# Kernel optimization log

Measured on AMD Instinct MI355X. Metric: run time of the kernel, lower is better.

## Reference

```python
import jax, jax.numpy as jnp
import numpy as np

B, S, D = 4, 2048, 1024
H, DK, DV = 16, 64, 64
EPS = 1e-6


def setup_inputs() -> dict:
    key = jax.random.key(0)
    ks = jax.random.split(key, 7)
    sc = 0.02
    return {
        "q": jax.random.normal(ks[0], (B, S, D), jnp.float32),
        "k": jax.random.normal(ks[1], (B, S, D), jnp.float32),
        "v": jax.random.normal(ks[2], (B, S, D), jnp.float32),
        "Wq": jax.random.normal(ks[3], (D, H * DK), jnp.float32) * sc,
        "Wk": jax.random.normal(ks[4], (D, H * DK), jnp.float32) * sc,
        "Wv": jax.random.normal(ks[5], (D, H * DV), jnp.float32) * sc,
        "Wo": jax.random.normal(ks[6], (H * DV, D), jnp.float32) * sc,
        "ln_gamma": jnp.ones((D,), jnp.float32),
        "ln_beta": jnp.zeros((D,), jnp.float32),
    }


def reference(q, k, v, Wq, Wk, Wv, Wo, ln_gamma, ln_beta):
    residual = q
    # QKV projections -> [b, h, s, d]
    qh = (q @ Wq).reshape(B, S, H, DK).transpose(0, 2, 1, 3)
    kh = (k @ Wk).reshape(B, S, H, DK).transpose(0, 2, 1, 3)
    vh = (v @ Wv).reshape(B, S, H, DV).transpose(0, 2, 1, 3)
    temperature = jnp.sqrt(jnp.float32(DK))
    # scaled dot-product attention (reverse=False, dropout = eval identity)
    scores = jnp.einsum('bhqd,bhkd->bhqk', qh / temperature, kh)
    attn = jax.nn.softmax(scores, axis=-1)
    ctx = jnp.einsum('bhqk,bhkd->bhqd', attn, vh)
    # merge heads and output projection
    ctx = ctx.transpose(0, 2, 1, 3).reshape(B, S, H * DV)
    out = ctx @ Wo + residual
    # LayerNorm eps=1e-6
    mu = out.mean(-1, keepdims=True)
    var = out.var(-1, keepdims=True)
    out = (out - mu) / jnp.sqrt(var + EPS) * ln_gamma + ln_beta
    return out
```

## Files before the change

kernel.cpp:

```cpp
#include <hip/hip_runtime.h>

typedef __bf16 bf16x8 __attribute__((ext_vector_type(8)));
typedef __bf16 bf16x4 __attribute__((ext_vector_type(4)));
typedef float  f32x4  __attribute__((ext_vector_type(4)));

#define MFMA16(a, b, c) __builtin_amdgcn_mfma_f32_16x16x32_bf16(a, b, c, 0, 0, 0)
#define AS1(p) ((__attribute__((address_space(1))) void*)(p))
#define AS3(p) ((__attribute__((address_space(3))) void*)(p))

union U8 { uint u[4]; bf16x8 v; };
union U4 { bf16x4 h[2]; bf16x8 v; };

__device__ inline uint packbf(float a, float b) {
  union { __bf16 h[2]; uint u; } x;
  x.h[0] = (__bf16)a; x.h[1] = (__bf16)b; return x.u;
}

__device__ inline float fast_exp2(float x) {
  float r;
  asm("v_exp_f32 %0, %1" : "=v"(r) : "v"(x));
  return r;
}

__global__ __launch_bounds__(256) void cvt3_kernel(const float* __restrict__ q,
                                                   const float* __restrict__ k,
                                                   const float* __restrict__ v,
                                                   __bf16* __restrict__ out, int n4) {
  const int z = blockIdx.y;
  const float* in = z == 0 ? q : (z == 1 ? k : v);
  int i = blockIdx.x * blockDim.x + threadIdx.x;
  if (i < n4) {
    float4 vv = ((const float4*)in)[i];
    bf16x4 o = {(__bf16)vv.x, (__bf16)vv.y, (__bf16)vv.z, (__bf16)vv.w};
    *(bf16x4*)(out + (size_t)z * n4 * 4 + (size_t)i * 4) = o;
  }
}

__global__ void wtrans_kernel(const float* __restrict__ in, __bf16* __restrict__ out) {
  __shared__ __bf16 t[64][65];
  int bx = blockIdx.x * 64, by = blockIdx.y * 64;
  int tx = threadIdx.x;
  for (int ty = threadIdx.y; ty < 64; ty += 4)
    t[ty][tx] = (__bf16)in[(size_t)(by + ty) * 1024 + bx + tx];
  __syncthreads();
  for (int ty = threadIdx.y; ty < 64; ty += 4)
    out[(size_t)(bx + ty) * 1024 + by + tx] = t[tx][ty];
}

__global__ __launch_bounds__(256) void gemm_qkv_kernel(
    const __bf16* __restrict__ A0, const __bf16* __restrict__ B0, __bf16* __restrict__ C0,
    const __bf16* __restrict__ A1, const __bf16* __restrict__ B1, __bf16* __restrict__ C1,
    const __bf16* __restrict__ A2, const __bf16* __restrict__ B2, __bf16* __restrict__ C2) {
  __shared__ __bf16 As[128 * 32];
  __shared__ __bf16 Bs[128 * 32];
  const int z = blockIdx.z;
  const __bf16* A = z == 0 ? A0 : (z == 1 ? A1 : A2);
  const __bf16* BT = z == 0 ? B0 : (z == 1 ? B1 : B2);
  __bf16* Cb = z == 0 ? C0 : (z == 1 ? C1 : C2);
  const int K = 1024, N = 1024;
  const int t = threadIdx.x, l = t & 63, w = t >> 6;
  const int lr = l & 15, lg = l >> 4;
  const int brow = blockIdx.y * 128, bcol = blockIdx.x * 128;
  const int wr = w >> 1, wc = w & 1;
  f32x4 acc[4][4] = {};

  const int srow = w * 16 + (l >> 2);
  const int scol = (l & 3) * 8;
  const __bf16* Ag = A + (size_t)(brow + srow) * K + scol;
  const __bf16* Bg = BT + (size_t)(bcol + srow) * K + scol;
  __bf16* Asw = As + w * 512;
  __bf16* Bsw = Bs + w * 512;

  for (int k0 = 0; k0 < K; k0 += 32) {
    __builtin_amdgcn_global_load_lds(AS1(Ag + k0), AS3(Asw), 16, 0, 0);
    __builtin_amdgcn_global_load_lds(AS1(Ag + k0 + (size_t)64 * K), AS3(Asw + 2048), 16, 0, 0);
    __builtin_amdgcn_global_load_lds(AS1(Bg + k0), AS3(Bsw), 16, 0, 0);
    __builtin_amdgcn_global_load_lds(AS1(Bg + k0 + (size_t)64 * K), AS3(Bsw + 2048), 16, 0, 0);
    __syncthreads();
    bf16x8 a[4], b[4];
#pragma unroll
    for (int m = 0; m < 4; ++m)
      a[m] = *(const bf16x8*)(As + (wr * 64 + m * 16 + lr) * 32 + lg * 8);
#pragma unroll
    for (int n = 0; n < 4; ++n)
      b[n] = *(const bf16x8*)(Bs + (wc * 64 + n * 16 + lr) * 32 + lg * 8);
#pragma unroll
    for (int m = 0; m < 4; ++m)
#pragma unroll
      for (int n = 0; n < 4; ++n)
        acc[m][n] = MFMA16(a[m], b[n], acc[m][n]);
    __syncthreads();
  }

  const int r0 = brow + wr * 64 + lg * 4;
  const int c0 = bcol + wc * 64 + lr;
  const float scale = (z == 0) ? 0.1803368801111244f : 1.0f;
#pragma unroll
  for (int m = 0; m < 4; ++m)
#pragma unroll
    for (int n = 0; n < 4; ++n) {
      if (z == 2) {
        const int dg = c0 + n * 16;
        const int tok = r0 + m * 16;
        bf16x4 pk4;
#pragma unroll
        for (int r = 0; r < 4; ++r) pk4[r] = (__bf16)acc[m][n][r];
        size_t idx = ((size_t)((tok >> 11) * 16 + (dg >> 6)) * 64 + (dg & 63)) * 2048 + (tok & 2047);
        *(bf16x4*)(Cb + idx) = pk4;
      } else {
#pragma unroll
        for (int r = 0; r < 4; ++r) {
          size_t idx = (size_t)(r0 + m * 16 + r) * N + c0 + n * 16;
          Cb[idx] = (__bf16)(acc[m][n][r] * scale);
        }
      }
    }
}

__global__ __launch_bounds__(256) void gemm_out_kernel(
    const __bf16* __restrict__ A, const __bf16* __restrict__ BT,
    float* __restrict__ Cf, const float* __restrict__ resid, int M, int N, int K) {
  __shared__ __bf16 As[128 * 32];
  __shared__ __bf16 Bs[128 * 32];
  const int t = threadIdx.x, l = t & 63, w = t >> 6;
  const int lr = l & 15, lg = l >> 4;
  const int brow = blockIdx.y * 128, bcol = blockIdx.x * 128;
  const int wr = w >> 1, wc = w & 1;
  f32x4 acc[4][4] = {};

  const int srow = w * 16 + (l >> 2);
  const int scol = (l & 3) * 8;
  const __bf16* Ag = A + (size_t)(brow + srow) * K + scol;
  const __bf16* Bg = BT + (size_t)(bcol + srow) * K + scol;
  __bf16* Asw = As + w * 512;
  __bf16* Bsw = Bs + w * 512;

  for (int k0 = 0; k0 < K; k0 += 32) {
    __builtin_amdgcn_global_load_lds(AS1(Ag + k0), AS3(Asw), 16, 0, 0);
    __builtin_amdgcn_global_load_lds(AS1(Ag + k0 + (size_t)64 * K), AS3(Asw + 2048), 16, 0, 0);
    __builtin_amdgcn_global_load_lds(AS1(Bg + k0), AS3(Bsw), 16, 0, 0);
    __builtin_amdgcn_global_load_lds(AS1(Bg + k0 + (size_t)64 * K), AS3(Bsw + 2048), 16, 0, 0);
    __syncthreads();
    bf16x8 a[4], b[4];
#pragma unroll
    for (int m = 0; m < 4; ++m)
      a[m] = *(const bf16x8*)(As + (wr * 64 + m * 16 + lr) * 32 + lg * 8);
#pragma unroll
    for (int n = 0; n < 4; ++n)
      b[n] = *(const bf16x8*)(Bs + (wc * 64 + n * 16 + lr) * 32 + lg * 8);
#pragma unroll
    for (int m = 0; m < 4; ++m)
#pragma unroll
      for (int n = 0; n < 4; ++n)
        acc[m][n] = MFMA16(a[m], b[n], acc[m][n]);
    __syncthreads();
  }

  const int r0 = brow + wr * 64 + lg * 4;
  const int c0 = bcol + wc * 64 + lr;
#pragma unroll
  for (int m = 0; m < 4; ++m)
#pragma unroll
    for (int n = 0; n < 4; ++n)
#pragma unroll
      for (int r = 0; r < 4; ++r) {
        size_t idx = (size_t)(r0 + m * 16 + r) * N + c0 + n * 16;
        Cf[idx] = acc[m][n][r] + resid[idx];
      }
}

__global__ __launch_bounds__(256) void attn_kernel(const __bf16* __restrict__ Qh,
                                                   const __bf16* __restrict__ Kh,
                                                   const __bf16* __restrict__ VhT,
                                                   __bf16* __restrict__ Ctx) {
  __shared__ __bf16 Vbuf[2 * 8192];
  const int t = threadIdx.x, l = t & 63, w = t >> 6;
  const int lr = l & 15, lg = l >> 4;
  const int bh = blockIdx.y;
  const size_t base = (size_t)(bh >> 4) * (2048 * 1024) + (size_t)(bh & 15) * 64;
  const int q0 = blockIdx.x * 128 + w * 32;

  bf16x8 aq[2][2];
#pragma unroll
  for (int nq = 0; nq < 2; ++nq)
#pragma unroll
    for (int kc = 0; kc < 2; ++kc)
      aq[nq][kc] = *(const bf16x8*)(Qh + base + (size_t)(q0 + nq * 16 + lr) * 1024 + kc * 32 + lg * 8);

  bf16x8 ones;
#pragma unroll
  for (int j = 0; j < 8; ++j) ones[j] = (__bf16)1.0f;

  f32x4 o[4][2] = {};
  f32x4 osum[2] = {};

  const int l8 = l & 7, lrow = l >> 3;
  const __bf16* vsrc = VhT + (size_t)bh * 131072 + (size_t)(w * 16 + lrow) * 2048 + ((l8 ^ lrow) * 8);

  const int xorm = (l8) << 4;
  int vo[2][2];
#pragma unroll
  for (int kc = 0; kc < 2; ++kc)
#pragma unroll
    for (int h = 0; h < 2; ++h)
      vo[kc][h] = lr * 128 + ((kc * 64 + h * 32 + lg * 8) ^ xorm);

#pragma unroll
  for (int h2 = 0; h2 < 2; ++h2) {
    __builtin_amdgcn_global_load_lds(AS1(vsrc + h2 * 64), AS3(Vbuf + h2 * 4096 + w * 1024), 16, 0, 0);
    __builtin_amdgcn_global_load_lds(AS1(vsrc + h2 * 64 + 16384), AS3(Vbuf + h2 * 4096 + w * 1024 + 512), 16, 0, 0);
  }
  __syncthreads();

  for (int tt = 0; tt < 16; ++tt) {
    const __bf16* Vcur = Vbuf + (tt & 1) * 8192;
    __bf16* Vn = Vbuf + ((tt + 1) & 1) * 8192;
    const int kvn = ((tt + 1) & 15) * 128;

#pragma unroll
    for (int h2 = 0; h2 < 2; ++h2) {
      __builtin_amdgcn_global_load_lds(AS1(vsrc + kvn + h2 * 64), AS3(Vn + h2 * 4096 + w * 1024), 16, 0, 0);
      __builtin_amdgcn_global_load_lds(AS1(vsrc + kvn + h2 * 64 + 16384), AS3(Vn + h2 * 4096 + w * 1024 + 512), 16, 0, 0);
    }

#pragma unroll
    for (int h2 = 0; h2 < 2; ++h2) {
      const int kv0 = tt * 128 + h2 * 64;
      const __bf16* Vb = Vcur + h2 * 4096;

      bf16x8 kf[4][2];
#pragma unroll
      for (int mkv = 0; mkv < 4; ++mkv)
#pragma unroll
        for (int kc = 0; kc < 2; ++kc)
          kf[mkv][kc] = *(const bf16x8*)(Kh + base + (size_t)(kv0 + mkv * 16 + lr) * 1024 + kc * 32 + lg * 8);

      f32x4 s[2][4];
      __builtin_amdgcn_s_setprio(1);
#pragma unroll
      for (int nq = 0; nq < 2; ++nq)
#pragma unroll
        for (int mkv = 0; mkv < 4; ++mkv) {
          f32x4 acc = {};
          acc = MFMA16(kf[mkv][0], aq[nq][0], acc);
          acc = MFMA16(kf[mkv][1], aq[nq][1], acc);
          s[nq][mkv] = acc;
        }
      __builtin_amdgcn_s_setprio(0);

      uint pk[2][4][2];
#pragma unroll
      for (int nq = 0; nq < 2; ++nq)
#pragma unroll
        for (int mkv = 0; mkv < 4; ++mkv) {
          float p0 = fast_exp2(s[nq][mkv][0]);
          float p1 = fast_exp2(s[nq][mkv][1]);
          float p2 = fast_exp2(s[nq][mkv][2]);
          float p3 = fast_exp2(s[nq][mkv][3]);
          pk[nq][mkv][0] = packbf(p0, p1);
          pk[nq][mkv][1] = packbf(p2, p3);
        }

      __builtin_amdgcn_s_setprio(1);
#pragma unroll
      for (int kc = 0; kc < 2; ++kc) {
        U8 pf[2];
#pragma unroll
        for (int nq = 0; nq < 2; ++nq) {
          pf[nq].u[0] = pk[nq][2 * kc][0];
          pf[nq].u[1] = pk[nq][2 * kc][1];
          pf[nq].u[2] = pk[nq][2 * kc + 1][0];
          pf[nq].u[3] = pk[nq][2 * kc + 1][1];
          osum[nq] = MFMA16(ones, pf[nq].v, osum[nq]);
        }
#pragma unroll
        for (int md = 0; md < 4; ++md) {
          U4 vf;
          vf.h[0] = *(const bf16x4*)((const char*)Vb + md * 2048 + vo[kc][0]);
          vf.h[1] = *(const bf16x4*)((const char*)Vb + md * 2048 + vo[kc][1]);
#pragma unroll
          for (int nq = 0; nq < 2; ++nq)
            o[md][nq] = MFMA16(vf.v, pf[nq].v, o[md][nq]);
        }
      }
      __builtin_amdgcn_s_setprio(0);
    }

    __syncthreads();
  }

  float rinv[2] = {1.f / osum[0][0], 1.f / osum[1][0]};
#pragma unroll
  for (int md = 0; md < 4; ++md)
#pragma unroll
    for (int nq = 0; nq < 2; ++nq) {
      bf16x4 pk4;
#pragma unroll
      for (int r = 0; r < 4; ++r) pk4[r] = (__bf16)(o[md][nq][r] * rinv[nq]);
      *(bf16x4*)(Ctx + base + (size_t)(q0 + nq * 16 + lr) * 1024 + md * 16 + lg * 4) = pk4;
    }
}

__global__ __launch_bounds__(256) void ln_kernel(const float* __restrict__ x,
                                                 const float* __restrict__ g,
                                                 const float* __restrict__ bta,
                                                 float* __restrict__ out) {
  __shared__ float sred[4], s2red[4];
  const int row = blockIdx.x, t = threadIdx.x;
  float4 v = ((const float4*)(x + (size_t)row * 1024))[t];
  float s = v.x + v.y + v.z + v.w;
  float s2 = v.x * v.x + v.y * v.y + v.z * v.z + v.w * v.w;
#pragma unroll
  for (int mask = 1; mask < 64; mask <<= 1) {
    s += __shfl_xor(s, mask);
    s2 += __shfl_xor(s2, mask);
  }
  if ((t & 63) == 0) { sred[t >> 6] = s; s2red[t >> 6] = s2; }
  __syncthreads();
  s = sred[0] + sred[1] + sred[2] + sred[3];
  s2 = s2red[0] + s2red[1] + s2red[2] + s2red[3];
  float mu = s * (1.f / 1024.f);
  float inv = rsqrtf(s2 * (1.f / 1024.f) - mu * mu + 1e-6f);
  float4 gv = ((const float4*)g)[t];
  float4 bv = ((const float4*)bta)[t];
  float4 ov;
  ov.x = (v.x - mu) * inv * gv.x + bv.x;
  ov.y = (v.y - mu) * inv * gv.y + bv.y;
  ov.z = (v.z - mu) * inv * gv.z + bv.z;
  ov.w = (v.w - mu) * inv * gv.w + bv.w;
  ((float4*)(out + (size_t)row * 1024))[t] = ov;
}

extern "C" void kernel_launch(void* const* d_in, const int* in_sizes, int n_in,
                              void* d_out, int out_size, void* d_ws, size_t ws_size,
                              hipStream_t stream) {
  const float* q  = (const float*)d_in[0];
  const float* k  = (const float*)d_in[1];
  const float* v  = (const float*)d_in[2];
  const float* Wq = (const float*)d_in[3];
  const float* Wk = (const float*)d_in[4];
  const float* Wv = (const float*)d_in[5];
  const float* Wo = (const float*)d_in[6];
  const float* g  = (const float*)d_in[7];
  const float* bt = (const float*)d_in[8];
  float* out = (float*)d_out;

  const int NTOK = 4 * 2048;
  const int NEL = NTOK * 1024;

  __bf16* qb  = (__bf16*)d_ws;
  __bf16* kb  = qb + NEL;
  __bf16* vb  = kb + NEL;
  __bf16* WqT = vb + NEL;
  __bf16* WkT = WqT + 1024 * 1024;
  __bf16* WvT = WkT + 1024 * 1024;
  __bf16* WoT = WvT + 1024 * 1024;
  __bf16* Qh  = WoT + 1024 * 1024;
  __bf16* Kh  = Qh + NEL;
  __bf16* VhT = Kh + NEL;
  __bf16* ctx = qb;
  float*  ao  = (float*)kb;

  cvt3_kernel<<<dim3(NEL / 1024, 3), 256, 0, stream>>>(q, k, v, qb, NEL / 4);

  dim3 wtb(64, 4), wtg(16, 16);
  wtrans_kernel<<<wtg, wtb, 0, stream>>>(Wq, WqT);
  wtrans_kernel<<<wtg, wtb, 0, stream>>>(Wk, WkT);
  wtrans_kernel<<<wtg, wtb, 0, stream>>>(Wv, WvT);
  wtrans_kernel<<<wtg, wtb, 0, stream>>>(Wo, WoT);

  gemm_qkv_kernel<<<dim3(1024 / 128, NTOK / 128, 3), 256, 0, stream>>>(
      qb, WqT, Qh, kb, WkT, Kh, vb, WvT, VhT);

  attn_kernel<<<dim3(2048 / 128, 64), 256, 0, stream>>>(Qh, Kh, VhT, ctx);

  gemm_out_kernel<<<dim3(1024 / 128, NTOK / 128), 256, 0, stream>>>(
      ctx, WoT, ao, q, NTOK, 1024, 1024);

  ln_kernel<<<NTOK, 256, 0, stream>>>(ao, g, bt, out);
}
```

Before: 444.4 us.

## Vectorize GEMM epilogues via swapped MFMA operands and widen attention blocks

The GEMM code moves into a templated body that, for the Q/K and output projections, swaps the MFMA operands so each lane holds four consecutive output columns. This lets the epilogue write packed bf16x4 and float4 stores and read the residual as float4, replacing scattered scalar stores. Separately, the attention kernel goes from 256 to 512 threads per block covering 256 queries, so each V tile loaded into LDS is shared by eight waves and each wave issues half as many V loads. The larger attention block may lower occupancy or raise register pressure.

```diff
diff --git a/kernel.cpp b/kernel.cpp
--- a/kernel.cpp
+++ b/kernel.cpp
@@ -47,6 +47,87 @@
     out[(size_t)(bx + ty) * 1024 + by + tx] = t[tx][ty];
 }
 
+template <int SWAP, int MODE>
+__device__ __forceinline__ void gemm_body(const __bf16* __restrict__ A,
+                                          const __bf16* __restrict__ BT,
+                                          __bf16* __restrict__ Cb,
+                                          float* __restrict__ Cf,
+                                          const float* __restrict__ resid,
+                                          float scale, __bf16* As, __bf16* Bs) {
+  const int K = 1024, N = 1024;
+  const int t = threadIdx.x, l = t & 63, w = t >> 6;
+  const int lr = l & 15, lg = l >> 4;
+  const int brow = blockIdx.y * 128, bcol = blockIdx.x * 128;
+  const int wr = w >> 1, wc = w & 1;
+  f32x4 acc[4][4] = {};
+
+  const int srow = w * 16 + (l >> 2);
+  const int scol = (l & 3) * 8;
+  const __bf16* Ag = A + (size_t)(brow + srow) * K + scol;
+  const __bf16* Bg = BT + (size_t)(bcol + srow) * K + scol;
+  __bf16* Asw = As + w * 512;
+  __bf16* Bsw = Bs + w * 512;
+
+  for (int k0 = 0; k0 < K; k0 += 32) {
+    __builtin_amdgcn_global_load_lds(AS1(Ag + k0), AS3(Asw), 16, 0, 0);
+    __builtin_amdgcn_global_load_lds(AS1(Ag + k0 + (size_t)64 * K), AS3(Asw + 2048), 16, 0, 0);
+    __builtin_amdgcn_global_load_lds(AS1(Bg + k0), AS3(Bsw), 16, 0, 0);
+    __builtin_amdgcn_global_load_lds(AS1(Bg + k0 + (size_t)64 * K), AS3(Bsw + 2048), 16, 0, 0);
+    __syncthreads();
+    bf16x8 a[4], b[4];
+#pragma unroll
+    for (int m = 0; m < 4; ++m)
+      a[m] = *(const bf16x8*)(As + (wr * 64 + m * 16 + lr) * 32 + lg * 8);
+#pragma unroll
+    for (int n = 0; n < 4; ++n)
+      b[n] = *(const bf16x8*)(Bs + (wc * 64 + n * 16 + lr) * 32 + lg * 8);
+#pragma unroll
+    for (int m = 0; m < 4; ++m)
+#pragma unroll
+      for (int n = 0; n < 4; ++n)
+        acc[m][n] = SWAP ? MFMA16(b[n], a[m], acc[m][n])
+                         : MFMA16(a[m], b[n], acc[m][n]);
+    __syncthreads();
+  }
+
+  if (MODE == 3) {
+    const int r0 = brow + wr * 64 + lg * 4;
+    const int c0 = bcol + wc * 64 + lr;
+#pragma unroll
+    for (int m = 0; m < 4; ++m)
+#pragma unroll
+      for (int n = 0; n < 4; ++n) {
+        const int dg = c0 + n * 16;
+        const int tok = r0 + m * 16;
+        bf16x4 pk4;
+#pragma unroll
+        for (int r = 0; r < 4; ++r) pk4[r] = (__bf16)acc[m][n][r];
+        size_t idx = ((size_t)((tok >> 11) * 16 + (dg >> 6)) * 64 + (dg & 63)) * 2048 + (tok & 2047);
+        *(bf16x4*)(Cb + idx) = pk4;
+      }
+  } else {
+    const int row0 = brow + wr * 64 + lr;
+    const int col0 = bcol + wc * 64 + lg * 4;
+#pragma unroll
+    for (int m = 0; m < 4; ++m)
+#pragma unroll
+      for (int n = 0; n < 4; ++n) {
+        size_t idx = (size_t)(row0 + m * 16) * N + col0 + n * 16;
+        if (MODE == 0) {
+          bf16x4 pk4;
+#pragma unroll
+          for (int r = 0; r < 4; ++r) pk4[r] = (__bf16)(acc[m][n][r] * scale);
+          *(bf16x4*)(Cb + idx) = pk4;
+        } else {
+          float4 rv = *(const float4*)(resid + idx);
+          float4 ov = {acc[m][n][0] + rv.x, acc[m][n][1] + rv.y,
+                       acc[m][n][2] + rv.z, acc[m][n][3] + rv.w};
+          *(float4*)(Cf + idx) = ov;
+        }
+      }
+  }
+}
+
 __global__ __launch_bounds__(256) void gemm_qkv_kernel(
     const __bf16* __restrict__ A0, const __bf16* __restrict__ B0, __bf16* __restrict__ C0,
     const __bf16* __restrict__ A1, const __bf16* __restrict__ B1, __bf16* __restrict__ C1,
@@ -54,122 +135,23 @@
   __shared__ __bf16 As[128 * 32];
   __shared__ __bf16 Bs[128 * 32];
   const int z = blockIdx.z;
-  const __bf16* A = z == 0 ? A0 : (z == 1 ? A1 : A2);
-  const __bf16* BT = z == 0 ? B0 : (z == 1 ? B1 : B2);
-  __bf16* Cb = z == 0 ? C0 : (z == 1 ? C1 : C2);
-  const int K = 1024, N = 1024;
-  const int t = threadIdx.x, l = t & 63, w = t >> 6;
-  const int lr = l & 15, lg = l >> 4;
-  const int brow = blockIdx.y * 128, bcol = blockIdx.x * 128;
-  const int wr = w >> 1, wc = w & 1;
-  f32x4 acc[4][4] = {};
-
-  const int srow = w * 16 + (l >> 2);
-  const int scol = (l & 3) * 8;
-  const __bf16* Ag = A + (size_t)(brow + srow) * K + scol;
-  const __bf16* Bg = BT + (size_t)(bcol + srow) * K + scol;
-  __bf16* Asw = As + w * 512;
-  __bf16* Bsw = Bs + w * 512;
-
-  for (int k0 = 0; k0 < K; k0 += 32) {
-    __builtin_amdgcn_global_load_lds(AS1(Ag + k0), AS3(Asw), 16, 0, 0);
-    __builtin_amdgcn_global_load_lds(AS1(Ag + k0 + (size_t)64 * K), AS3(Asw + 2048), 16, 0, 0);
-    __builtin_amdgcn_global_load_lds(AS1(Bg + k0), AS3(Bsw), 16, 0, 0);
-    __builtin_amdgcn_global_load_lds(AS1(Bg + k0 + (size_t)64 * K), AS3(Bsw + 2048), 16, 0, 0);
-    __syncthreads();
-    bf16x8 a[4], b[4];
-#pragma unroll
-    for (int m = 0; m < 4; ++m)
-      a[m] = *(const bf16x8*)(As + (wr * 64 + m * 16 + lr) * 32 + lg * 8);
-#pragma unroll
-    for (int n = 0; n < 4; ++n)
-      b[n] = *(const bf16x8*)(Bs + (wc * 64 + n * 16 + lr) * 32 + lg * 8);
-#pragma unroll
-    for (int m = 0; m < 4; ++m)
-#pragma unroll
-      for (int n = 0; n < 4; ++n)
-        acc[m][n] = MFMA16(a[m], b[n], acc[m][n]);
-    __syncthreads();
-  }
-
-  const int r0 = brow + wr * 64 + lg * 4;
-  const int c0 = bcol + wc * 64 + lr;
-  const float scale = (z == 0) ? 0.1803368801111244f : 1.0f;
-#pragma unroll
-  for (int m = 0; m < 4; ++m)
-#pragma unroll
-    for (int n = 0; n < 4; ++n) {
-      if (z == 2) {
-        const int dg = c0 + n * 16;
-        const int tok = r0 + m * 16;
-        bf16x4 pk4;
-#pragma unroll
-        for (int r = 0; r < 4; ++r) pk4[r] = (__bf16)acc[m][n][r];
-        size_t idx = ((size_t)((tok >> 11) * 16 + (dg >> 6)) * 64 + (dg & 63)) * 2048 + (tok & 2047);
-        *(bf16x4*)(Cb + idx) = pk4;
-      } else {
-#pragma unroll
-        for (int r = 0; r < 4; ++r) {
-          size_t idx = (size_t)(r0 + m * 16 + r) * N + c0 + n * 16;
-          Cb[idx] = (__bf16)(acc[m][n][r] * scale);
-        }
-      }
-    }
+  if (z == 2)
+    gemm_body<0, 3>(A2, B2, C2, nullptr, nullptr, 1.0f, As, Bs);
+  else if (z == 0)
+    gemm_body<1, 0>(A0, B0, C0, nullptr, nullptr, 0.1803368801111244f, As, Bs);
+  else
+    gemm_body<1, 0>(A1, B1, C1, nullptr, nullptr, 1.0f, As, Bs);
 }
 
 __global__ __launch_bounds__(256) void gemm_out_kernel(
     const __bf16* __restrict__ A, const __bf16* __restrict__ BT,
-    float* __restrict__ Cf, const float* __restrict__ resid, int M, int N, int K) {
+    float* __restrict__ Cf, const float* __restrict__ resid) {
   __shared__ __bf16 As[128 * 32];
   __shared__ __bf16 Bs[128 * 32];
-  const int t = threadIdx.x, l = t & 63, w = t >> 6;
-  const int lr = l & 15, lg = l >> 4;
-  const int brow = blockIdx.y * 128, bcol = blockIdx.x * 128;
-  const int wr = w >> 1, wc = w & 1;
-  f32x4 acc[4][4] = {};
-
-  const int srow = w * 16 + (l >> 2);
-  const int scol = (l & 3) * 8;
-  const __bf16* Ag = A + (size_t)(brow + srow) * K + scol;
-  const __bf16* Bg = BT + (size_t)(bcol + srow) * K + scol;
-  __bf16* Asw = As + w * 512;
-  __bf16* Bsw = Bs + w * 512;
-
-  for (int k0 = 0; k0 < K; k0 += 32) {
-    __builtin_amdgcn_global_load_lds(AS1(Ag + k0), AS3(Asw), 16, 0, 0);
-    __builtin_amdgcn_global_load_lds(AS1(Ag + k0 + (size_t)64 * K), AS3(Asw + 2048), 16, 0, 0);
-    __builtin_amdgcn_global_load_lds(AS1(Bg + k0), AS3(Bsw), 16, 0, 0);
-    __builtin_amdgcn_global_load_lds(AS1(Bg + k0 + (size_t)64 * K), AS3(Bsw + 2048), 16, 0, 0);
-    __syncthreads();
-    bf16x8 a[4], b[4];
-#pragma unroll
-    for (int m = 0; m < 4; ++m)
-      a[m] = *(const bf16x8*)(As + (wr * 64 + m * 16 + lr) * 32 + lg * 8);
-#pragma unroll
-    for (int n = 0; n < 4; ++n)
-      b[n] = *(const bf16x8*)(Bs + (wc * 64 + n * 16 + lr) * 32 + lg * 8);
-#pragma unroll
-    for (int m = 0; m < 4; ++m)
-#pragma unroll
-      for (int n = 0; n < 4; ++n)
-        acc[m][n] = MFMA16(a[m], b[n], acc[m][n]);
-    __syncthreads();
-  }
-
-  const int r0 = brow + wr * 64 + lg * 4;
-  const int c0 = bcol + wc * 64 + lr;
-#pragma unroll
-  for (int m = 0; m < 4; ++m)
-#pragma unroll
-    for (int n = 0; n < 4; ++n)
-#pragma unroll
-      for (int r = 0; r < 4; ++r) {
-        size_t idx = (size_t)(r0 + m * 16 + r) * N + c0 + n * 16;
-        Cf[idx] = acc[m][n][r] + resid[idx];
-      }
-}
-
-__global__ __launch_bounds__(256) void attn_kernel(const __bf16* __restrict__ Qh,
+  gemm_body<1, 1>(A, BT, nullptr, Cf, resid, 1.0f, As, Bs);
+}
+
+__global__ __launch_bounds__(512) void attn_kernel(const __bf16* __restrict__ Qh,
                                                    const __bf16* __restrict__ Kh,
                                                    const __bf16* __restrict__ VhT,
                                                    __bf16* __restrict__ Ctx) {
@@ -178,7 +160,7 @@
   const int lr = l & 15, lg = l >> 4;
   const int bh = blockIdx.y;
   const size_t base = (size_t)(bh >> 4) * (2048 * 1024) + (size_t)(bh & 15) * 64;
-  const int q0 = blockIdx.x * 128 + w * 32;
+  const int q0 = blockIdx.x * 256 + w * 32;
 
   bf16x8 aq[2][2];
 #pragma unroll
@@ -195,7 +177,7 @@
   f32x4 osum[2] = {};
 
   const int l8 = l & 7, lrow = l >> 3;
-  const __bf16* vsrc = VhT + (size_t)bh * 131072 + (size_t)(w * 16 + lrow) * 2048 + ((l8 ^ lrow) * 8);
+  const __bf16* vsrc = VhT + (size_t)bh * 131072 + (size_t)(w * 8 + lrow) * 2048 + ((l8 ^ lrow) * 8);
 
   const int xorm = (l8) << 4;
   int vo[2][2];
@@ -206,10 +188,8 @@
       vo[kc][h] = lr * 128 + ((kc * 64 + h * 32 + lg * 8) ^ xorm);
 
 #pragma unroll
-  for (int h2 = 0; h2 < 2; ++h2) {
-    __builtin_amdgcn_global_load_lds(AS1(vsrc + h2 * 64), AS3(Vbuf + h2 * 4096 + w * 1024), 16, 0, 0);
-    __builtin_amdgcn_global_load_lds(AS1(vsrc + h2 * 64 + 16384), AS3(Vbuf + h2 * 4096 + w * 1024 + 512), 16, 0, 0);
-  }
+  for (int h2 = 0; h2 < 2; ++h2)
+    __builtin_amdgcn_global_load_lds(AS1(vsrc + h2 * 64), AS3(Vbuf + h2 * 4096 + w * 512), 16, 0, 0);
   __syncthreads();
 
   for (int tt = 0; tt < 16; ++tt) {
@@ -218,10 +198,8 @@
     const int kvn = ((tt + 1) & 15) * 128;
 
 #pragma unroll
-    for (int h2 = 0; h2 < 2; ++h2) {
-      __builtin_amdgcn_global_load_lds(AS1(vsrc + kvn + h2 * 64), AS3(Vn + h2 * 4096 + w * 1024), 16, 0, 0);
-      __builtin_amdgcn_global_load_lds(AS1(vsrc + kvn + h2 * 64 + 16384), AS3(Vn + h2 * 4096 + w * 1024 + 512), 16, 0, 0);
-    }
+    for (int h2 = 0; h2 < 2; ++h2)
+      __builtin_amdgcn_global_load_lds(AS1(vsrc + kvn + h2 * 64), AS3(Vn + h2 * 4096 + w * 512), 16, 0, 0);
 
 #pragma unroll
     for (int h2 = 0; h2 < 2; ++h2) {
@@ -372,10 +350,9 @@
   gemm_qkv_kernel<<<dim3(1024 / 128, NTOK / 128, 3), 256, 0, stream>>>(
       qb, WqT, Qh, kb, WkT, Kh, vb, WvT, VhT);
 
-  attn_kernel<<<dim3(2048 / 128, 64), 256, 0, stream>>>(Qh, Kh, VhT, ctx);
-
-  gemm_out_kernel<<<dim3(1024 / 128, NTOK / 128), 256, 0, stream>>>(
-      ctx, WoT, ao, q, NTOK, 1024, 1024);
+  attn_kernel<<<dim3(2048 / 256, 64), 512, 0, stream>>>(Qh, Kh, VhT, ctx);
+
+  gemm_out_kernel<<<dim3(1024 / 128, NTOK / 128), 256, 0, stream>>>(ctx, WoT, ao, q);
 
   ln_kernel<<<NTOK, 256, 0, stream>>>(ao, g, bt, out);
 }
```

Measured after the change: 443.3 us. No clear change (-0.2%).
